# Performance work log

Hardware: AMD Instinct MI355X
Metric: run time of the kernel (lower is better)

Reference implementation:

```python
import jax, jax.numpy as jnp
import numpy as np

B, N, D, H = 4, 1024, 512, 8
DH = D // H  # per-head dim for V and for each of the two Q/K halves
LAM = 0.5


def setup_inputs() -> dict:
    key = jax.random.key(0)
    ks = jax.random.split(key, 7)
    s = 0.02
    return {
        "x": jax.random.normal(ks[0], (B, N, D), dtype=jnp.float32),
        "Wq": jax.random.normal(ks[1], (D, 2 * D), dtype=jnp.float32) * s,
        "bq": jax.random.normal(ks[2], (2 * D,), dtype=jnp.float32) * s,
        "Wk": jax.random.normal(ks[3], (D, 2 * D), dtype=jnp.float32) * s,
        "bk": jax.random.normal(ks[4], (2 * D,), dtype=jnp.float32) * s,
        "Wv": jax.random.normal(ks[5], (D, D), dtype=jnp.float32) * s,
        "bv": jax.random.normal(ks[6], (D,), dtype=jnp.float32) * s,
    }


def reference(x, Wq, bq, Wk, bk, Wv, bv):
    b, n, d = x.shape
    q = (x @ Wq + bq).reshape(b, n, H, 2 * DH).transpose(0, 2, 1, 3)  # [B,H,N,2*DH]
    k = (x @ Wk + bk).reshape(b, n, H, 2 * DH).transpose(0, 2, 1, 3)
    v = (x @ Wv + bv).reshape(b, n, H, DH).transpose(0, 2, 1, 3)      # [B,H,N,DH]
    q1, q2 = q[..., :DH], q[..., DH:]
    k1, k2 = k[..., :DH], k[..., DH:]
    scale = 1.0 / jnp.sqrt(jnp.float32(DH))
    a1 = jax.nn.softmax(jnp.einsum("bhqd,bhkd->bhqk", q1, k1) * scale, axis=-1)
    a2 = jax.nn.softmax(jnp.einsum("bhqd,bhkd->bhqk", q2, k2) * scale, axis=-1)
    attn = a1 - LAM * a2                                              # [B,H,N,N]
    out = jnp.einsum("bhqk,bhkd->bhqd", attn, v)                      # [B,H,N,DH]
    return out.transpose(0, 2, 1, 3).reshape(b, n, d)
```

## Files before the change

### kernel.cpp

```cpp
#include <hip/hip_runtime.h>
#include <hip/hip_bf16.h>

typedef unsigned short u16;
typedef unsigned int u32;
typedef short s16x8 __attribute__((ext_vector_type(8)));
typedef short s16x4 __attribute__((ext_vector_type(4)));
typedef float f32x4 __attribute__((ext_vector_type(4)));
typedef float f32x16 __attribute__((ext_vector_type(16)));

__device__ inline u16 f2bf(float f) {
  union { float f; unsigned int u; } v; v.f = f;
  unsigned int r = v.u + 0x7fffu + ((v.u >> 16) & 1u);
  return (u16)(r >> 16);
}

__device__ __forceinline__ u32 cvt_pk_bf16(float lo, float hi) {
  u32 r;
  asm("v_cvt_pk_bf16_f32 %0, %1, %2" : "=v"(r) : "v"(lo), "v"(hi));
  return r;
}

__device__ __forceinline__ void g2lds16(const u16* g, u16* l) {
  __builtin_amdgcn_global_load_lds((const __attribute__((address_space(1))) void*)g,
                                   (__attribute__((address_space(3))) void*)l, 16, 0, 0);
}

__global__ __launch_bounds__(256) void cast_x_kernel(const float* __restrict__ x,
                                                     u16* __restrict__ xb) {
  int i = (blockIdx.x * 256 + threadIdx.x) * 8;
  float4 a = *(const float4*)(x + i);
  float4 b = *(const float4*)(x + i + 4);
  s16x8 o;
  o[0] = (short)f2bf(a.x); o[1] = (short)f2bf(a.y);
  o[2] = (short)f2bf(a.z); o[3] = (short)f2bf(a.w);
  o[4] = (short)f2bf(b.x); o[5] = (short)f2bf(b.y);
  o[6] = (short)f2bf(b.z); o[7] = (short)f2bf(b.w);
  *(s16x8*)(xb + i) = o;
}

__global__ __launch_bounds__(256) void transpose_cast_w_all(const float* __restrict__ Wq,
                                                            const float* __restrict__ Wk,
                                                            const float* __restrict__ Wv,
                                                            u16* __restrict__ wt) {
  __shared__ float tile[64][65];
  int jg = blockIdx.x * 64;
  const float* src; int C, j0;
  if (jg < 1024)      { src = Wq; C = 1024; j0 = jg; }
  else if (jg < 2048) { src = Wk; C = 1024; j0 = jg - 1024; }
  else                { src = Wv; C = 512;  j0 = jg - 2048; }
  int k0 = blockIdx.y * 64;
  int tx = threadIdx.x % 64, ty4 = threadIdx.x / 64;
#pragma unroll
  for (int p = 0; p < 16; ++p) {
    int r = p * 4 + ty4;
    tile[r][tx] = src[(size_t)(k0 + r) * C + j0 + tx];
  }
  __syncthreads();
#pragma unroll
  for (int p = 0; p < 16; ++p) {
    int r = p * 4 + ty4;
    wt[(size_t)(jg + r) * 512 + k0 + tx] = f2bf(tile[tx][r]);
  }
}

__global__ __launch_bounds__(256, 2) void gemm_qkv(const u16* __restrict__ xb, const u16* __restrict__ wt,
                                                   const float* __restrict__ bq, const float* __restrict__ bk,
                                                   const float* __restrict__ bv,
                                                   u16* __restrict__ qa, u16* __restrict__ ka,
                                                   u16* __restrict__ va) {
  __shared__ __align__(16) u16 As[128 * 64];
  __shared__ __align__(16) u16 Bs[128 * 64];
  int m0 = blockIdx.x * 128, j0 = blockIdx.y * 128;
  int tid = threadIdx.x;
  int w = tid >> 6, lane = tid & 63, quad = lane >> 4, l16 = lane & 15;
  int wr = (w >> 1) * 64, wc = (w & 1) * 64;

  int srow[4], scol[4], sbase[4];
#pragma unroll
  for (int it = 0; it < 4; ++it) {
    int s = it * 256 + tid;
    srow[it] = s >> 3;
    scol[it] = (s & 7) ^ ((s >> 3) & 7);
    sbase[it] = (s & ~63) * 8;
  }

  f32x4 acc[4][4];
#pragma unroll
  for (int i = 0; i < 4; ++i)
#pragma unroll
    for (int j = 0; j < 4; ++j)
#pragma unroll
      for (int r = 0; r < 4; ++r) acc[i][j][r] = 0.f;

  for (int kk = 0; kk < 8; ++kk) {
    int k0 = kk * 64;
    __syncthreads();
#pragma unroll
    for (int it = 0; it < 4; ++it) {
      g2lds16(xb + (size_t)(m0 + srow[it]) * 512 + k0 + scol[it] * 8, &As[sbase[it]]);
      g2lds16(wt + (size_t)(j0 + srow[it]) * 512 + k0 + scol[it] * 8, &Bs[sbase[it]]);
    }
    __syncthreads();
#pragma unroll
    for (int kb = 0; kb < 2; ++kb) {
      s16x8 af[4], bfr[4];
#pragma unroll
      for (int rb = 0; rb < 4; ++rb) {
        int row = wr + rb * 16 + l16;
        af[rb] = *(const s16x8*)(&As[row * 64 + (((kb * 4 + quad) ^ (row & 7)) * 8)]);
      }
#pragma unroll
      for (int cb = 0; cb < 4; ++cb) {
        int row = wc + cb * 16 + l16;
        bfr[cb] = *(const s16x8*)(&Bs[row * 64 + (((kb * 4 + quad) ^ (row & 7)) * 8)]);
      }
#pragma unroll
      for (int rb = 0; rb < 4; ++rb)
#pragma unroll
        for (int cb = 0; cb < 4; ++cb)
          acc[rb][cb] = __builtin_amdgcn_mfma_f32_16x16x32_bf16(af[rb], bfr[cb], acc[rb][cb], 0, 0, 0);
    }
  }

#pragma unroll
  for (int cb = 0; cb < 4; ++cb) {
    int j = j0 + wc + cb * 16 + l16;
    float bias = (j < 1024) ? bq[j] : (j < 2048) ? bk[j - 1024] : bv[j - 2048];
#pragma unroll
    for (int rb = 0; rb < 4; ++rb) {
#pragma unroll
      for (int r = 0; r < 4; ++r) {
        int m = m0 + wr + rb * 16 + quad * 4 + r;
        int bidx = m >> 10, n = m & 1023;
        u16 o = f2bf(acc[rb][cb][r] + bias);
        if (j < 1024) {
          int h = j >> 7, r2 = j & 127;
          qa[((size_t)((bidx * 8 + h) * 1024 + n)) * 128 + r2] = o;
        } else if (j < 2048) {
          int jj = j - 1024, h = jj >> 7, r2 = jj & 127;
          ka[((size_t)((bidx * 8 + h) * 1024 + n)) * 128 + r2] = o;
        } else {
          int jj = j - 2048, h = jj >> 6, d = jj & 63;
          va[((size_t)((bidx * 8 + h) * 64 + d)) * 1024 + n] = o;
        }
      }
    }
  }
}

__global__ __launch_bounds__(256, 2) void attn_kernel(const u16* __restrict__ qa, const u16* __restrict__ ka,
                                                      const u16* __restrict__ va, float* __restrict__ out) {
  __shared__ __align__(16) u16 smem[40960];
  int bh = blockIdx.x, b = bh >> 3, h = bh & 7;
  int q0 = blockIdx.y * 64;
  int tid = threadIdx.x, w = tid >> 6, lane = tid & 63;
  int l32 = lane & 31, hi = lane >> 5;
  int team = w >> 1, wq = w & 1, t = tid & 127;
  u16* hb = smem + team * 20480;
  u16* const KbA = hb;
  u16* const KbB = hb + 8192;
  u16* const Vsb = hb + 16384;

  const u16* qrow = qa + (size_t)(bh * 1024 + q0 + wq * 32 + l32) * 128;
  s16x8 qf[2][4];
#pragma unroll
  for (int hh = 0; hh < 2; ++hh)
#pragma unroll
    for (int kb = 0; kb < 4; ++kb)
      qf[hh][kb] = *(const s16x8*)(qrow + 64 * hh + 16 * kb + 8 * hi);

  f32x16 O1[2], O2[2];
#pragma unroll
  for (int d = 0; d < 2; ++d)
#pragma unroll
    for (int r = 0; r < 16; ++r) { O1[d][r] = 0.f; O2[d][r] = 0.f; }
  float ds1 = 0.f, ds2 = 0.f;

  int r0 = t >> 4, c0 = t & 15;
  int rv = t >> 3, cv = (t & 7) ^ ((t >> 3) & 7);
  const u16* kgbase = ka + (size_t)bh * 1024 * 128;
  const u16* vgbase = va + (size_t)bh * 64 * 1024;
  int nbase = team * 512;

  auto stageK = [&](int n0, u16* Kd) {
#pragma unroll
    for (int it = 0; it < 8; ++it) {
      int row = r0 + 8 * it;
      int chunk = c0 ^ (row & 15);
      g2lds16(kgbase + (size_t)(n0 + row) * 128 + chunk * 8, Kd + (it * 128 + (t & 64)) * 8);
    }
  };
  auto stageV = [&](int n0) {
#pragma unroll
    for (int it = 0; it < 4; ++it)
      g2lds16(vgbase + (size_t)(rv + 16 * it) * 1024 + n0 + cv * 8, Vsb + (it * 128 + (t & 64)) * 8);
  };

  stageK(nbase, KbA);
  stageV(nbase);
  __syncthreads();

  for (int kt = 0; kt < 8; ++kt) {
    u16* const KsC = (kt & 1) ? KbB : KbA;
    u16* const KsN = (kt & 1) ? KbA : KbB;
    if (kt < 7) stageK(nbase + (kt + 1) * 64, KsN);

    s16x8 pa[2][4];
#pragma unroll
    for (int hh = 0; hh < 2; ++hh) {
      f32x16 sv[2];
#pragma unroll
      for (int nb = 0; nb < 2; ++nb)
#pragma unroll
        for (int r = 0; r < 16; ++r) sv[nb][r] = 0.f;
#pragma unroll
      for (int nb = 0; nb < 2; ++nb) {
        int row = nb * 32 + l32, rbase = row * 128, rx15 = row & 15;
#pragma unroll
        for (int kb = 0; kb < 4; ++kb) {
          s16x8 kf = *(const s16x8*)(&KsC[rbase + (((8 * hh + 2 * kb + hi) ^ rx15) * 8)]);
          sv[nb] = __builtin_amdgcn_mfma_f32_32x32x16_bf16(kf, qf[hh][kb], sv[nb], 0, 0, 0);
        }
      }
      float dsl = 0.f;
#pragma unroll
      for (int s = 0; s < 4; ++s) {
        float e[8];
#pragma unroll
        for (int j = 0; j < 8; ++j) {
          e[j] = __builtin_exp2f(sv[s >> 1][(s & 1) * 8 + j] * 0.18033688f);
          dsl += e[j];
        }
        union { u32 wd[4]; s16x8 v; } u;
        u.wd[0] = cvt_pk_bf16(e[0], e[1]);
        u.wd[1] = cvt_pk_bf16(e[2], e[3]);
        u.wd[2] = cvt_pk_bf16(e[4], e[5]);
        u.wd[3] = cvt_pk_bf16(e[6], e[7]);
        pa[hh][s] = u.v;
      }
      if (hh == 0) ds1 += dsl; else ds2 += dsl;
    }

    s16x8 vB[4][2];
#pragma unroll
    for (int dblk = 0; dblk < 2; ++dblk) {
      int row = dblk * 32 + l32, rbase = row * 64, rx = row & 7;
#pragma unroll
      for (int s = 0; s < 4; ++s) {
        union { s16x4 hl[2]; s16x8 v; } u;
        u.hl[0] = *(const s16x4*)(&Vsb[rbase + (((2 * s) ^ rx) * 8) + 4 * hi]);
        u.hl[1] = *(const s16x4*)(&Vsb[rbase + (((2 * s + 1) ^ rx) * 8) + 4 * hi]);
        vB[s][dblk] = u.v;
      }
    }

    asm volatile("s_waitcnt lgkmcnt(0)\n\ts_barrier" ::: "memory");
    if (kt < 7) stageV(nbase + (kt + 1) * 64);

#pragma unroll
    for (int s = 0; s < 4; ++s)
#pragma unroll
      for (int dblk = 0; dblk < 2; ++dblk) {
        O1[dblk] = __builtin_amdgcn_mfma_f32_32x32x16_bf16(pa[0][s], vB[s][dblk], O1[dblk], 0, 0, 0);
        O2[dblk] = __builtin_amdgcn_mfma_f32_32x32x16_bf16(pa[1][s], vB[s][dblk], O2[dblk], 0, 0, 0);
      }

    __syncthreads();
  }

  float* scr = (float*)smem;
  int mbase = wq * 4224 + lane;
  if (team == 1) {
#pragma unroll
    for (int r = 0; r < 16; ++r) {
      scr[mbase + r * 64]        = O1[0][r];
      scr[mbase + (16 + r) * 64] = O1[1][r];
      scr[mbase + (32 + r) * 64] = O2[0][r];
      scr[mbase + (48 + r) * 64] = O2[1][r];
    }
    scr[mbase + 64 * 64] = ds1;
    scr[mbase + 65 * 64] = ds2;
  }
  __syncthreads();
  if (team == 0) {
#pragma unroll
    for (int r = 0; r < 16; ++r) {
      O1[0][r] += scr[mbase + r * 64];
      O1[1][r] += scr[mbase + (16 + r) * 64];
      O2[0][r] += scr[mbase + (32 + r) * 64];
      O2[1][r] += scr[mbase + (48 + r) * 64];
    }
    ds1 += scr[mbase + 64 * 64];
    ds2 += scr[mbase + 65 * 64];
    ds1 += __shfl_xor(ds1, 32, 64);
    ds2 += __shfl_xor(ds2, 32, 64);
    float inv1 = 1.0f / ds1, inv2 = 1.0f / ds2;
#pragma unroll
    for (int r = 0; r < 16; ++r) {
      int iq = (r & 3) + 8 * (r >> 2) + 4 * hi;
      float i1 = __shfl(inv1, iq, 64);
      float i2 = __shfl(inv2, iq, 64);
      size_t orow = (size_t)(b * 1024 + q0 + wq * 32 + iq) * 512 + h * 64 + l32;
      out[orow]      = O1[0][r] * i1 - 0.5f * O2[0][r] * i2;
      out[orow + 32] = O1[1][r] * i1 - 0.5f * O2[1][r] * i2;
    }
  }
}

extern "C" void kernel_launch(void* const* d_in, const int* in_sizes, int n_in,
                              void* d_out, int out_size, void* d_ws, size_t ws_size,
                              hipStream_t stream) {
  (void)in_sizes; (void)n_in; (void)out_size; (void)ws_size;
  const float* x  = (const float*)d_in[0];
  const float* Wq = (const float*)d_in[1];
  const float* bq = (const float*)d_in[2];
  const float* Wk = (const float*)d_in[3];
  const float* bk = (const float*)d_in[4];
  const float* Wv = (const float*)d_in[5];
  const float* bv = (const float*)d_in[6];
  float* out = (float*)d_out;

  char* ws = (char*)d_ws;
  u16* xb = (u16*)(ws);
  u16* wt = (u16*)(ws + 4194304);
  u16* qa = (u16*)(ws + 6815744);
  u16* ka = (u16*)(ws + 15204352);
  u16* va = (u16*)(ws + 23592960);

  cast_x_kernel<<<1024, 256, 0, stream>>>(x, xb);
  transpose_cast_w_all<<<dim3(40, 8), 256, 0, stream>>>(Wq, Wk, Wv, wt);
  gemm_qkv<<<dim3(32, 20), 256, 0, stream>>>(xb, wt, bq, bk, bv, qa, ka, va);
  attn_kernel<<<dim3(32, 16), 256, 0, stream>>>(qa, ka, va, out);
}
```

Measured before the change: 134.5 us.

## Load K and V fragments directly from global memory instead of LDS staging

Removes the double-buffered LDS staging of K and V tiles, along with the per-iteration barriers, and has each wave read its MFMA operand fragments straight from global memory (relying on cache). This drops LDS traffic and synchronisation and shrinks shared memory to just the reduction scratch, which may allow higher occupancy. In exchange, the two waves of a team now each fetch the same K/V data redundantly, there is no async prefetch overlap, and the V reads are strided 8-byte accesses across rows 1024 elements apart.

```diff
diff --git a/kernel.cpp b/kernel.cpp
--- a/kernel.cpp
+++ b/kernel.cpp
@@ -150,16 +150,12 @@
 
 __global__ __launch_bounds__(256, 2) void attn_kernel(const u16* __restrict__ qa, const u16* __restrict__ ka,
                                                       const u16* __restrict__ va, float* __restrict__ out) {
-  __shared__ __align__(16) u16 smem[40960];
+  __shared__ float scr[8448];
   int bh = blockIdx.x, b = bh >> 3, h = bh & 7;
   int q0 = blockIdx.y * 64;
   int tid = threadIdx.x, w = tid >> 6, lane = tid & 63;
   int l32 = lane & 31, hi = lane >> 5;
-  int team = w >> 1, wq = w & 1, t = tid & 127;
-  u16* hb = smem + team * 20480;
-  u16* const KbA = hb;
-  u16* const KbB = hb + 8192;
-  u16* const Vsb = hb + 16384;
+  int team = w >> 1, wq = w & 1;
 
   const u16* qrow = qa + (size_t)(bh * 1024 + q0 + wq * 32 + l32) * 128;
   s16x8 qf[2][4];
@@ -176,34 +172,12 @@
     for (int r = 0; r < 16; ++r) { O1[d][r] = 0.f; O2[d][r] = 0.f; }
   float ds1 = 0.f, ds2 = 0.f;
 
-  int r0 = t >> 4, c0 = t & 15;
-  int rv = t >> 3, cv = (t & 7) ^ ((t >> 3) & 7);
-  const u16* kgbase = ka + (size_t)bh * 1024 * 128;
-  const u16* vgbase = va + (size_t)bh * 64 * 1024;
-  int nbase = team * 512;
-
-  auto stageK = [&](int n0, u16* Kd) {
-#pragma unroll
-    for (int it = 0; it < 8; ++it) {
-      int row = r0 + 8 * it;
-      int chunk = c0 ^ (row & 15);
-      g2lds16(kgbase + (size_t)(n0 + row) * 128 + chunk * 8, Kd + (it * 128 + (t & 64)) * 8);
-    }
-  };
-  auto stageV = [&](int n0) {
-#pragma unroll
-    for (int it = 0; it < 4; ++it)
-      g2lds16(vgbase + (size_t)(rv + 16 * it) * 1024 + n0 + cv * 8, Vsb + (it * 128 + (t & 64)) * 8);
-  };
-
-  stageK(nbase, KbA);
-  stageV(nbase);
-  __syncthreads();
+  const u16* kg = ka + (size_t)bh * 1024 * 128 + (size_t)team * 512 * 128;
+  const u16* vg = va + (size_t)bh * 64 * 1024 + team * 512;
 
   for (int kt = 0; kt < 8; ++kt) {
-    u16* const KsC = (kt & 1) ? KbB : KbA;
-    u16* const KsN = (kt & 1) ? KbA : KbB;
-    if (kt < 7) stageK(nbase + (kt + 1) * 64, KsN);
+    const u16* kt0 = kg + kt * 64 * 128;
+    const u16* vt0 = vg + kt * 64;
 
     s16x8 pa[2][4];
 #pragma unroll
@@ -215,10 +189,10 @@
         for (int r = 0; r < 16; ++r) sv[nb][r] = 0.f;
 #pragma unroll
       for (int nb = 0; nb < 2; ++nb) {
-        int row = nb * 32 + l32, rbase = row * 128, rx15 = row & 15;
+        const u16* krow = kt0 + (size_t)(nb * 32 + l32) * 128 + 8 * hi;
 #pragma unroll
         for (int kb = 0; kb < 4; ++kb) {
-          s16x8 kf = *(const s16x8*)(&KsC[rbase + (((8 * hh + 2 * kb + hi) ^ rx15) * 8)]);
+          s16x8 kf = *(const s16x8*)(krow + (8 * hh + 2 * kb) * 8);
           sv[nb] = __builtin_amdgcn_mfma_f32_32x32x16_bf16(kf, qf[hh][kb], sv[nb], 0, 0, 0);
         }
       }
@@ -244,18 +218,15 @@
     s16x8 vB[4][2];
 #pragma unroll
     for (int dblk = 0; dblk < 2; ++dblk) {
-      int row = dblk * 32 + l32, rbase = row * 64, rx = row & 7;
+      const u16* vrow = vt0 + (size_t)(dblk * 32 + l32) * 1024 + 4 * hi;
 #pragma unroll
       for (int s = 0; s < 4; ++s) {
         union { s16x4 hl[2]; s16x8 v; } u;
-        u.hl[0] = *(const s16x4*)(&Vsb[rbase + (((2 * s) ^ rx) * 8) + 4 * hi]);
-        u.hl[1] = *(const s16x4*)(&Vsb[rbase + (((2 * s + 1) ^ rx) * 8) + 4 * hi]);
+        u.hl[0] = *(const s16x4*)(vrow + 16 * s);
+        u.hl[1] = *(const s16x4*)(vrow + 16 * s + 8);
         vB[s][dblk] = u.v;
       }
     }
-
-    asm volatile("s_waitcnt lgkmcnt(0)\n\ts_barrier" ::: "memory");
-    if (kt < 7) stageV(nbase + (kt + 1) * 64);
 
 #pragma unroll
     for (int s = 0; s < 4; ++s)
@@ -264,11 +235,8 @@
         O1[dblk] = __builtin_amdgcn_mfma_f32_32x32x16_bf16(pa[0][s], vB[s][dblk], O1[dblk], 0, 0, 0);
         O2[dblk] = __builtin_amdgcn_mfma_f32_32x32x16_bf16(pa[1][s], vB[s][dblk], O2[dblk], 0, 0, 0);
       }
-
-    __syncthreads();
-  }
-
-  float* scr = (float*)smem;
+  }
+
   int mbase = wq * 4224 + lane;
   if (team == 1) {
 #pragma unroll
```

Result: slower. 162.2 us (+20.6%).
